# Optimization experiments

Measured on AMD Instinct MI355X. Metric: run time of the kernel, lower is better.

Reference implementation:

```python
import jax, jax.numpy as jnp
import numpy as np

B = 128
E, IN, H, OUT, ZD = 6, 1664, 512, 618, 32


def setup_inputs() -> dict:
    key = jax.random.key(0)
    ks = jax.random.split(key, 9)
    scale = 0.05
    return {
        "p_prev": jax.random.normal(ks[0], (B, IN), dtype=jnp.float32),
        "blending_coef": jax.random.uniform(ks[1], (B, E), dtype=jnp.float32),
        "z": jax.random.normal(ks[2], (B, ZD), dtype=jnp.float32),
        "w_l1": jax.random.normal(ks[3], (E, IN, H), dtype=jnp.float32) * scale,
        "b_l1": jax.random.normal(ks[4], (E, H), dtype=jnp.float32) * scale,
        "w_l2": jax.random.normal(ks[5], (E, H + ZD, H), dtype=jnp.float32) * scale,
        "b_l2": jax.random.normal(ks[6], (E, H + ZD, H)[0:0] + (E, H), dtype=jnp.float32) * scale,
        "w_l3": jax.random.normal(ks[7], (E, H + ZD, OUT), dtype=jnp.float32) * scale,
        "b_l3": jax.random.normal(ks[8], (E, OUT), dtype=jnp.float32) * scale,
    }


def _moe_layer(x, coef, w, b, use_act=True):
    # Per-sample blended weight matmul, fused as a single contraction:
    # y[b,o] = sum_i x[b,i] * (sum_e coef[b,e] * w[e,i,o]) + sum_e coef[b,e] * b[e,o]
    y = jnp.einsum("bi,eio,be->bo", x, w, coef) + jnp.einsum("be,eo->bo", coef, b)
    return jax.nn.elu(y) if use_act else y


def reference(p_prev, blending_coef, z, w_l1, b_l1, w_l2, b_l2, w_l3, b_l3):
    x = _moe_layer(p_prev, blending_coef, w_l1, b_l1)              # [B, H]
    x = _moe_layer(jnp.concatenate([x, z], axis=-1), blending_coef, w_l2, b_l2)  # [B, H]
    x = _moe_layer(jnp.concatenate([x, z], axis=-1), blending_coef, w_l3, b_l3, use_act=False)  # [B, OUT]
    return x
```

## Files before the change

### kernel.cpp

```cpp
#include <hip/hip_runtime.h>
#include <math.h>

#define B 128
#define E 6
#define IN_DIM 1664
#define H_DIM 512
#define OUT_DIM 618
#define ZD 32
#define K2 544
#define S1 26
#define S23 17

typedef __attribute__((ext_vector_type(8))) short short8;
typedef __attribute__((ext_vector_type(4))) float f32x4;
union U128 { uint4 u4; short8 s8; ushort us[8]; };

__device__ __forceinline__ ushort f2bf(float f) {
    uint u = __float_as_uint(f);
    u += 0x7fffu + ((u >> 16) & 1u);
    return (ushort)(u >> 16);
}
__device__ __forceinline__ uint pk2(float a, float b) {
    return (uint)f2bf(a) | ((uint)f2bf(b) << 16);
}
__device__ __forceinline__ float elu1(float x) { return x < 0.f ? expm1f(x) : x; }


__global__ __launch_bounds__(256) void init_bias(
    const float* __restrict__ coef,
    const float* __restrict__ b1, const float* __restrict__ b2,
    const float* __restrict__ b3,
    float* __restrict__ y1, float* __restrict__ y2, float* __restrict__ out)
{
    const int idx = blockIdx.x * 256 + threadIdx.x;
    if (idx >= B * (2 * H_DIM + OUT_DIM)) return;
    const int b = idx / (2 * H_DIM + OUT_DIM);
    const int o = idx - b * (2 * H_DIM + OUT_DIM);
    float ce[E];
    #pragma unroll
    for (int e = 0; e < E; ++e) ce[e] = coef[b * E + e];
    float v = 0.f;
    if (o < H_DIM) {
        #pragma unroll
        for (int e = 0; e < E; ++e) v = fmaf(ce[e], b1[e * H_DIM + o], v);
        y1[b * H_DIM + o] = v;
    } else if (o < 2 * H_DIM) {
        const int oo = o - H_DIM;
        #pragma unroll
        for (int e = 0; e < E; ++e) v = fmaf(ce[e], b2[e * H_DIM + oo], v);
        y2[b * H_DIM + oo] = v;
    } else {
        const int oo = o - 2 * H_DIM;
        #pragma unroll
        for (int e = 0; e < E; ++e) v = fmaf(ce[e], b3[e * OUT_DIM + oo], v);
        out[b * OUT_DIM + oo] = v;
    }
}

__global__ __launch_bounds__(256) void gemm1(
    const float* __restrict__ x,
    const float* __restrict__ coef,
    const float* __restrict__ w,
    float* __restrict__ y1)
{
    constexpr int NS = E * 2;
    const int tid = threadIdx.x;
    const int l = tid & 63, wv = tid >> 6;
    const int n0 = blockIdx.x * 16, kb0 = blockIdx.y * 2;
    const int tn = tid & 15, tq = tid >> 4;
    const int lp = ((tq >> 2) << 4) | tn;
    const int j0 = (2 * tq) & 7;
    const int row0 = 32 * wv + (l & 15), row1 = row0 + 16, kq = l >> 4;

    __shared__ ushort bs[NS][64][8];

    float wreg[NS][2];
    #pragma unroll
    for (int s = 0; s < NS; ++s) {
        const int e = s % E, kb = kb0 + s / E;
        const float* src = w + ((size_t)e * IN_DIM + kb * 32 + 2 * tq) * H_DIM + n0 + tn;
        wreg[s][0] = src[0];
        wreg[s][1] = src[H_DIM];
    }
    float4 xreg[2][4];
    #pragma unroll
    for (int kbi = 0; kbi < 2; ++kbi) {
        const float* p0 = x + (size_t)row0 * IN_DIM + (kb0 + kbi) * 32 + kq * 8;
        const float* p1 = x + (size_t)row1 * IN_DIM + (kb0 + kbi) * 32 + kq * 8;
        xreg[kbi][0] = *reinterpret_cast<const float4*>(p0);
        xreg[kbi][1] = *reinterpret_cast<const float4*>(p0 + 4);
        xreg[kbi][2] = *reinterpret_cast<const float4*>(p1);
        xreg[kbi][3] = *reinterpret_cast<const float4*>(p1 + 4);
    }
    float ce0[E], ce1[E];
    #pragma unroll
    for (int e = 0; e < E; ++e) {
        ce0[e] = coef[row0 * E + e];
        ce1[e] = coef[row1 * E + e];
    }

    #pragma unroll
    for (int s = 0; s < NS; ++s)
        *reinterpret_cast<uint*>(&bs[s][lp][j0]) = pk2(wreg[s][0], wreg[s][1]);
    __syncthreads();

    f32x4 acc0 = {0.f,0.f,0.f,0.f}, acc1 = {0.f,0.f,0.f,0.f};
    #pragma unroll
    for (int s = 0; s < NS; ++s) {
        const int e = s % E, kbi = s / E;
        const float4* xc = xreg[kbi];
        U128 a0, a1;
        a0.us[0] = f2bf(xc[0].x * ce0[e]); a0.us[1] = f2bf(xc[0].y * ce0[e]);
        a0.us[2] = f2bf(xc[0].z * ce0[e]); a0.us[3] = f2bf(xc[0].w * ce0[e]);
        a0.us[4] = f2bf(xc[1].x * ce0[e]); a0.us[5] = f2bf(xc[1].y * ce0[e]);
        a0.us[6] = f2bf(xc[1].z * ce0[e]); a0.us[7] = f2bf(xc[1].w * ce0[e]);
        a1.us[0] = f2bf(xc[2].x * ce1[e]); a1.us[1] = f2bf(xc[2].y * ce1[e]);
        a1.us[2] = f2bf(xc[2].z * ce1[e]); a1.us[3] = f2bf(xc[2].w * ce1[e]);
        a1.us[4] = f2bf(xc[3].x * ce1[e]); a1.us[5] = f2bf(xc[3].y * ce1[e]);
        a1.us[6] = f2bf(xc[3].z * ce1[e]); a1.us[7] = f2bf(xc[3].w * ce1[e]);

        U128 b0;
        b0.u4 = *reinterpret_cast<const uint4*>(&bs[s][l][0]);
        acc0 = __builtin_amdgcn_mfma_f32_16x16x32_bf16(a0.s8, b0.s8, acc0, 0, 0, 0);
        acc1 = __builtin_amdgcn_mfma_f32_16x16x32_bf16(a1.s8, b0.s8, acc1, 0, 0, 0);
    }

    const int colB = n0 + (l & 15);
    const int rsub = (l >> 4) << 2;
    #pragma unroll
    for (int mi = 0; mi < 2; ++mi) {
        const int row = wv * 32 + mi * 16 + rsub;
        const f32x4 c = mi ? acc1 : acc0;
        #pragma unroll
        for (int r = 0; r < 4; ++r)
            atomicAdd(&y1[(size_t)(row + r) * H_DIM + colB], c[r]);
    }
}

template<bool ZS, int NW, bool GUARD>
__device__ __forceinline__ void gemm_mid_body(
    const float* __restrict__ yin,
    const float* __restrict__ coef,
    const float* __restrict__ z,
    const float* __restrict__ w,
    float* __restrict__ yout,
    int nt, int kb0, ushort (*bs)[64][8])
{
    constexpr int NS = E;
    const int tid = threadIdx.x;
    const int l = tid & 63, wv = tid >> 6;
    const int n0 = nt * 16;
    const int tn = tid & 15, tq = tid >> 4;
    const int lp = ((tq >> 2) << 4) | tn;
    const int j0 = (2 * tq) & 7;
    const int row0 = 32 * wv + (l & 15), row1 = row0 + 16, kq = l >> 4;
    const bool okS = !GUARD || (n0 + tn) < NW;
    const bool okC = !GUARD || (n0 + (l & 15)) < NW;

    float wreg[NS][2];
    #pragma unroll
    for (int s = 0; s < NS; ++s) {
        const float* src = w + ((size_t)s * K2 + kb0 * 32 + 2 * tq) * NW + n0 + tn;
        wreg[s][0] = okS ? src[0] : 0.f;
        wreg[s][1] = okS ? src[NW] : 0.f;
    }

    float ce0[E], ce1[E];
    #pragma unroll
    for (int e = 0; e < E; ++e) {
        ce0[e] = coef[row0 * E + e];
        ce1[e] = coef[row1 * E + e];
    }

    float v0[8], v1[8];
    if (ZS) {
        const float4 za = *reinterpret_cast<const float4*>(z + row0 * ZD + kq * 8);
        const float4 zb = *reinterpret_cast<const float4*>(z + row0 * ZD + kq * 8 + 4);
        const float4 zc = *reinterpret_cast<const float4*>(z + row1 * ZD + kq * 8);
        const float4 zd = *reinterpret_cast<const float4*>(z + row1 * ZD + kq * 8 + 4);
        v0[0]=za.x; v0[1]=za.y; v0[2]=za.z; v0[3]=za.w;
        v0[4]=zb.x; v0[5]=zb.y; v0[6]=zb.z; v0[7]=zb.w;
        v1[0]=zc.x; v1[1]=zc.y; v1[2]=zc.z; v1[3]=zc.w;
        v1[4]=zd.x; v1[5]=zd.y; v1[6]=zd.z; v1[7]=zd.w;
    } else {
        const int kk = kb0 * 32 + kq * 8;
        const float* p0 = yin + (size_t)row0 * H_DIM + kk;
        const float* p1 = yin + (size_t)row1 * H_DIM + kk;
        const float4 a = *reinterpret_cast<const float4*>(p0);
        const float4 b = *reinterpret_cast<const float4*>(p0 + 4);
        const float4 c = *reinterpret_cast<const float4*>(p1);
        const float4 d = *reinterpret_cast<const float4*>(p1 + 4);
        v0[0]=elu1(a.x); v0[1]=elu1(a.y); v0[2]=elu1(a.z); v0[3]=elu1(a.w);
        v0[4]=elu1(b.x); v0[5]=elu1(b.y); v0[6]=elu1(b.z); v0[7]=elu1(b.w);
        v1[0]=elu1(c.x); v1[1]=elu1(c.y); v1[2]=elu1(c.z); v1[3]=elu1(c.w);
        v1[4]=elu1(d.x); v1[5]=elu1(d.y); v1[6]=elu1(d.z); v1[7]=elu1(d.w);
    }

    #pragma unroll
    for (int s = 0; s < NS; ++s)
        *reinterpret_cast<uint*>(&bs[s][lp][j0]) = pk2(wreg[s][0], wreg[s][1]);
    __syncthreads();

    f32x4 acc0 = {0.f,0.f,0.f,0.f}, acc1 = {0.f,0.f,0.f,0.f};
    #pragma unroll
    for (int s = 0; s < NS; ++s) {
        U128 a0, a1;
        #pragma unroll
        for (int j = 0; j < 8; ++j) {
            a0.us[j] = f2bf(v0[j] * ce0[s]);
            a1.us[j] = f2bf(v1[j] * ce1[s]);
        }
        U128 b0;
        b0.u4 = *reinterpret_cast<const uint4*>(&bs[s][l][0]);
        acc0 = __builtin_amdgcn_mfma_f32_16x16x32_bf16(a0.s8, b0.s8, acc0, 0, 0, 0);
        acc1 = __builtin_amdgcn_mfma_f32_16x16x32_bf16(a1.s8, b0.s8, acc1, 0, 0, 0);
    }

    const int colB = n0 + (l & 15);
    const int rsub = (l >> 4) << 2;
    #pragma unroll
    for (int mi = 0; mi < 2; ++mi) {
        const int row = wv * 32 + mi * 16 + rsub;
        const f32x4 c = mi ? acc1 : acc0;
        #pragma unroll
        for (int r = 0; r < 4; ++r)
            if (okC) atomicAdd(&yout[(size_t)(row + r) * NW + colB], c[r]);
    }
}

__global__ __launch_bounds__(256) void gemm_l2(
    const float* __restrict__ y1, const float* __restrict__ coef,
    const float* __restrict__ z, const float* __restrict__ w2,
    float* __restrict__ y2)
{
    __shared__ ushort bs[E][64][8];
    const int nt = blockIdx.x, sp = blockIdx.y;
    if (sp < 16)
        gemm_mid_body<false, H_DIM, false>(y1, coef, z, w2, y2, nt, sp, bs);
    else
        gemm_mid_body<true, H_DIM, false>(y1, coef, z, w2, y2, nt, 16, bs);
}

__global__ __launch_bounds__(256) void gemm_l3(
    const float* __restrict__ y2, const float* __restrict__ coef,
    const float* __restrict__ z, const float* __restrict__ w3,
    float* __restrict__ out)
{
    __shared__ ushort bs[E][64][8];
    const int nt = blockIdx.x, sp = blockIdx.y;
    if (sp < 16)
        gemm_mid_body<false, OUT_DIM, true>(y2, coef, z, w3, out, nt, sp, bs);
    else
        gemm_mid_body<true, OUT_DIM, true>(y2, coef, z, w3, out, nt, 16, bs);
}

extern "C" void kernel_launch(void* const* d_in, const int* in_sizes, int n_in,
                              void* d_out, int out_size, void* d_ws, size_t ws_size,
                              hipStream_t stream)
{
    const float* p_prev = (const float*)d_in[0];
    const float* coef   = (const float*)d_in[1];
    const float* z      = (const float*)d_in[2];
    const float* w1     = (const float*)d_in[3];
    const float* b1     = (const float*)d_in[4];
    const float* w2     = (const float*)d_in[5];
    const float* b2     = (const float*)d_in[6];
    const float* w3     = (const float*)d_in[7];
    const float* b3     = (const float*)d_in[8];
    float* out = (float*)d_out;

    float* y1 = (float*)d_ws;
    float* y2 = y1 + (size_t)B * H_DIM;

    const int TOT = B * (2 * H_DIM + OUT_DIM);
    init_bias<<<(TOT + 255) / 256, 256, 0, stream>>>(coef, b1, b2, b3, y1, y2, out);
    gemm1<<<dim3(32, S1), 256, 0, stream>>>(p_prev, coef, w1, y1);
    gemm_l2<<<dim3(32, S23), 256, 0, stream>>>(y1, coef, z, w2, y2);
    gemm_l3<<<dim3(39, S23), 256, 0, stream>>>(y2, coef, z, w3, out);
}
```

Before: 47.21 us.

## Split batch rows across blocks, deepen K per block, fold bias init into gemm1

Each block now covers 64 batch rows instead of all 128, with one MFMA chain per wave, and handles more K slices per block (4 k-blocks in gemm1, 2 in layers 2 and 3). This halves the split-K fan-out of atomics per output while doubling the column-tile grid. Bias init for y2 and out moves into an extra row of gemm1 blocks, leaving a small vectorized init kernel for y1. The trade-off is that each weight tile is now loaded twice (once per row half), which raises weight traffic, and each block uses more registers for the deeper K slice.

```diff
diff --git a/kernel.cpp b/kernel.cpp
--- a/kernel.cpp
+++ b/kernel.cpp
@@ -8,8 +8,6 @@
 #define OUT_DIM 618
 #define ZD 32
 #define K2 544
-#define S1 26
-#define S23 17
 
 typedef __attribute__((ext_vector_type(8))) short short8;
 typedef __attribute__((ext_vector_type(4))) float f32x4;
@@ -26,205 +24,188 @@
 __device__ __forceinline__ float elu1(float x) { return x < 0.f ? expm1f(x) : x; }
 
 
-__global__ __launch_bounds__(256) void init_bias(
-    const float* __restrict__ coef,
-    const float* __restrict__ b1, const float* __restrict__ b2,
-    const float* __restrict__ b3,
-    float* __restrict__ y1, float* __restrict__ y2, float* __restrict__ out)
-{
-    const int idx = blockIdx.x * 256 + threadIdx.x;
-    if (idx >= B * (2 * H_DIM + OUT_DIM)) return;
-    const int b = idx / (2 * H_DIM + OUT_DIM);
-    const int o = idx - b * (2 * H_DIM + OUT_DIM);
-    float ce[E];
-    #pragma unroll
-    for (int e = 0; e < E; ++e) ce[e] = coef[b * E + e];
-    float v = 0.f;
-    if (o < H_DIM) {
-        #pragma unroll
-        for (int e = 0; e < E; ++e) v = fmaf(ce[e], b1[e * H_DIM + o], v);
-        y1[b * H_DIM + o] = v;
-    } else if (o < 2 * H_DIM) {
-        const int oo = o - H_DIM;
-        #pragma unroll
-        for (int e = 0; e < E; ++e) v = fmaf(ce[e], b2[e * H_DIM + oo], v);
-        y2[b * H_DIM + oo] = v;
-    } else {
-        const int oo = o - 2 * H_DIM;
-        #pragma unroll
-        for (int e = 0; e < E; ++e) v = fmaf(ce[e], b3[e * OUT_DIM + oo], v);
-        out[b * OUT_DIM + oo] = v;
-    }
+__global__ __launch_bounds__(256) void init_y1(
+    const float* __restrict__ coef, const float* __restrict__ b1,
+    float* __restrict__ y1)
+{
+    const int t = blockIdx.x * 256 + threadIdx.x;
+    const int b = t >> 7, o = (t & 127) << 2;
+    float4 v = {0.f, 0.f, 0.f, 0.f};
+    #pragma unroll
+    for (int e = 0; e < E; ++e) {
+        const float c = coef[b * E + e];
+        const float4 bb = *reinterpret_cast<const float4*>(b1 + e * H_DIM + o);
+        v.x = fmaf(c, bb.x, v.x); v.y = fmaf(c, bb.y, v.y);
+        v.z = fmaf(c, bb.z, v.z); v.w = fmaf(c, bb.w, v.w);
+    }
+    *reinterpret_cast<float4*>(y1 + b * H_DIM + o) = v;
 }
 
 __global__ __launch_bounds__(256) void gemm1(
     const float* __restrict__ x,
     const float* __restrict__ coef,
     const float* __restrict__ w,
-    float* __restrict__ y1)
-{
-    constexpr int NS = E * 2;
+    const float* __restrict__ b2, const float* __restrict__ b3,
+    float* __restrict__ y1, float* __restrict__ y2, float* __restrict__ out)
+{
+    __shared__ ushort bs[24][64][8];
     const int tid = threadIdx.x;
+
+    if (blockIdx.y == 0) {
+        const int t = blockIdx.x * 256 + tid;
+        {
+            const int b = t >> 7, o = (t & 127) << 2;
+            float4 v = {0.f, 0.f, 0.f, 0.f};
+            #pragma unroll
+            for (int e = 0; e < E; ++e) {
+                const float c = coef[b * E + e];
+                const float4 bb = *reinterpret_cast<const float4*>(b2 + e * H_DIM + o);
+                v.x = fmaf(c, bb.x, v.x); v.y = fmaf(c, bb.y, v.y);
+                v.z = fmaf(c, bb.z, v.z); v.w = fmaf(c, bb.w, v.w);
+            }
+            *reinterpret_cast<float4*>(y2 + b * H_DIM + o) = v;
+        }
+        for (int i = t; i < B * OUT_DIM; i += 64 * 256) {
+            const int b = i / OUT_DIM, o = i - b * OUT_DIM;
+            float v = 0.f;
+            #pragma unroll
+            for (int e = 0; e < E; ++e)
+                v = fmaf(coef[b * E + e], b3[e * OUT_DIM + o], v);
+            out[i] = v;
+        }
+        return;
+    }
+
+    const int kb0 = (blockIdx.y - 1) * 4;
+    const int n0 = (blockIdx.x & 31) * 16, rowbase = (blockIdx.x >> 5) * 64;
     const int l = tid & 63, wv = tid >> 6;
-    const int n0 = blockIdx.x * 16, kb0 = blockIdx.y * 2;
     const int tn = tid & 15, tq = tid >> 4;
-    const int lp = ((tq >> 2) << 4) | tn;
-    const int j0 = (2 * tq) & 7;
-    const int row0 = 32 * wv + (l & 15), row1 = row0 + 16, kq = l >> 4;
-
-    __shared__ ushort bs[NS][64][8];
-
-    float wreg[NS][2];
-    #pragma unroll
-    for (int s = 0; s < NS; ++s) {
-        const int e = s % E, kb = kb0 + s / E;
-        const float* src = w + ((size_t)e * IN_DIM + kb * 32 + 2 * tq) * H_DIM + n0 + tn;
-        wreg[s][0] = src[0];
-        wreg[s][1] = src[H_DIM];
-    }
-    float4 xreg[2][4];
-    #pragma unroll
-    for (int kbi = 0; kbi < 2; ++kbi) {
-        const float* p0 = x + (size_t)row0 * IN_DIM + (kb0 + kbi) * 32 + kq * 8;
-        const float* p1 = x + (size_t)row1 * IN_DIM + (kb0 + kbi) * 32 + kq * 8;
-        xreg[kbi][0] = *reinterpret_cast<const float4*>(p0);
-        xreg[kbi][1] = *reinterpret_cast<const float4*>(p0 + 4);
-        xreg[kbi][2] = *reinterpret_cast<const float4*>(p1);
-        xreg[kbi][3] = *reinterpret_cast<const float4*>(p1 + 4);
-    }
-    float ce0[E], ce1[E];
-    #pragma unroll
-    for (int e = 0; e < E; ++e) {
-        ce0[e] = coef[row0 * E + e];
-        ce1[e] = coef[row1 * E + e];
-    }
-
-    #pragma unroll
-    for (int s = 0; s < NS; ++s)
-        *reinterpret_cast<uint*>(&bs[s][lp][j0]) = pk2(wreg[s][0], wreg[s][1]);
+    const int lp = ((tq >> 2) << 4) | tn, j0 = (2 * tq) & 7;
+    const int row = rowbase + wv * 16 + (l & 15);
+    const int kq = l >> 4;
+
+    float ce[E];
+    #pragma unroll
+    for (int e = 0; e < E; ++e) ce[e] = coef[row * E + e];
+
+    float xv[4][8];
+    #pragma unroll
+    for (int kbi = 0; kbi < 4; ++kbi) {
+        const float* p = x + (size_t)row * IN_DIM + (kb0 + kbi) * 32 + kq * 8;
+        const float4 a = *reinterpret_cast<const float4*>(p);
+        const float4 b = *reinterpret_cast<const float4*>(p + 4);
+        xv[kbi][0] = a.x; xv[kbi][1] = a.y; xv[kbi][2] = a.z; xv[kbi][3] = a.w;
+        xv[kbi][4] = b.x; xv[kbi][5] = b.y; xv[kbi][6] = b.z; xv[kbi][7] = b.w;
+    }
+
+    #pragma unroll
+    for (int bb = 0; bb < 2; ++bb) {
+        float wr[12][2];
+        #pragma unroll
+        for (int ss = 0; ss < 12; ++ss) {
+            const int s = bb * 12 + ss;
+            const int e = s % E, kb = kb0 + s / E;
+            const float* src = w + ((size_t)e * IN_DIM + kb * 32 + 2 * tq) * H_DIM + n0 + tn;
+            wr[ss][0] = src[0];
+            wr[ss][1] = src[H_DIM];
+        }
+        #pragma unroll
+        for (int ss = 0; ss < 12; ++ss)
+            *reinterpret_cast<uint*>(&bs[bb * 12 + ss][lp][j0]) =
+                pk2(wr[ss][0], wr[ss][1]);
+    }
     __syncthreads();
 
-    f32x4 acc0 = {0.f,0.f,0.f,0.f}, acc1 = {0.f,0.f,0.f,0.f};
-    #pragma unroll
-    for (int s = 0; s < NS; ++s) {
+    f32x4 acc = {0.f, 0.f, 0.f, 0.f};
+    #pragma unroll
+    for (int s = 0; s < 24; ++s) {
         const int e = s % E, kbi = s / E;
-        const float4* xc = xreg[kbi];
-        U128 a0, a1;
-        a0.us[0] = f2bf(xc[0].x * ce0[e]); a0.us[1] = f2bf(xc[0].y * ce0[e]);
-        a0.us[2] = f2bf(xc[0].z * ce0[e]); a0.us[3] = f2bf(xc[0].w * ce0[e]);
-        a0.us[4] = f2bf(xc[1].x * ce0[e]); a0.us[5] = f2bf(xc[1].y * ce0[e]);
-        a0.us[6] = f2bf(xc[1].z * ce0[e]); a0.us[7] = f2bf(xc[1].w * ce0[e]);
-        a1.us[0] = f2bf(xc[2].x * ce1[e]); a1.us[1] = f2bf(xc[2].y * ce1[e]);
-        a1.us[2] = f2bf(xc[2].z * ce1[e]); a1.us[3] = f2bf(xc[2].w * ce1[e]);
-        a1.us[4] = f2bf(xc[3].x * ce1[e]); a1.us[5] = f2bf(xc[3].y * ce1[e]);
-        a1.us[6] = f2bf(xc[3].z * ce1[e]); a1.us[7] = f2bf(xc[3].w * ce1[e]);
-
-        U128 b0;
+        U128 a, b0;
+        #pragma unroll
+        for (int j = 0; j < 8; ++j) a.us[j] = f2bf(xv[kbi][j] * ce[e]);
         b0.u4 = *reinterpret_cast<const uint4*>(&bs[s][l][0]);
-        acc0 = __builtin_amdgcn_mfma_f32_16x16x32_bf16(a0.s8, b0.s8, acc0, 0, 0, 0);
-        acc1 = __builtin_amdgcn_mfma_f32_16x16x32_bf16(a1.s8, b0.s8, acc1, 0, 0, 0);
+        acc = __builtin_amdgcn_mfma_f32_16x16x32_bf16(a.s8, b0.s8, acc, 0, 0, 0);
     }
 
     const int colB = n0 + (l & 15);
-    const int rsub = (l >> 4) << 2;
-    #pragma unroll
-    for (int mi = 0; mi < 2; ++mi) {
-        const int row = wv * 32 + mi * 16 + rsub;
-        const f32x4 c = mi ? acc1 : acc0;
-        #pragma unroll
-        for (int r = 0; r < 4; ++r)
-            atomicAdd(&y1[(size_t)(row + r) * H_DIM + colB], c[r]);
-    }
-}
-
-template<bool ZS, int NW, bool GUARD>
+    const int rowE = rowbase + wv * 16 + ((l >> 4) << 2);
+    #pragma unroll
+    for (int r = 0; r < 4; ++r)
+        atomicAdd(&y1[(size_t)(rowE + r) * H_DIM + colB], acc[r]);
+}
+
+template<int KPB, bool ZS, int NW, bool GUARD>
 __device__ __forceinline__ void gemm_mid_body(
     const float* __restrict__ yin,
     const float* __restrict__ coef,
     const float* __restrict__ z,
     const float* __restrict__ w,
     float* __restrict__ yout,
-    int nt, int kb0, ushort (*bs)[64][8])
-{
-    constexpr int NS = E;
+    int n0, int rowbase, int kb0, ushort (*bs)[64][8])
+{
+    constexpr int NS = E * KPB;
     const int tid = threadIdx.x;
     const int l = tid & 63, wv = tid >> 6;
-    const int n0 = nt * 16;
     const int tn = tid & 15, tq = tid >> 4;
-    const int lp = ((tq >> 2) << 4) | tn;
-    const int j0 = (2 * tq) & 7;
-    const int row0 = 32 * wv + (l & 15), row1 = row0 + 16, kq = l >> 4;
+    const int lp = ((tq >> 2) << 4) | tn, j0 = (2 * tq) & 7;
+    const int row = rowbase + wv * 16 + (l & 15);
+    const int kq = l >> 4;
     const bool okS = !GUARD || (n0 + tn) < NW;
-    const bool okC = !GUARD || (n0 + (l & 15)) < NW;
-
-    float wreg[NS][2];
+
+    float wr[NS][2];
     #pragma unroll
     for (int s = 0; s < NS; ++s) {
-        const float* src = w + ((size_t)s * K2 + kb0 * 32 + 2 * tq) * NW + n0 + tn;
-        wreg[s][0] = okS ? src[0] : 0.f;
-        wreg[s][1] = okS ? src[NW] : 0.f;
-    }
-
-    float ce0[E], ce1[E];
-    #pragma unroll
-    for (int e = 0; e < E; ++e) {
-        ce0[e] = coef[row0 * E + e];
-        ce1[e] = coef[row1 * E + e];
-    }
-
-    float v0[8], v1[8];
+        const int e = s % E, kb = kb0 + s / E;
+        const float* src = w + ((size_t)e * K2 + kb * 32 + 2 * tq) * NW + n0 + tn;
+        wr[s][0] = okS ? src[0] : 0.f;
+        wr[s][1] = okS ? src[NW] : 0.f;
+    }
+
+    float ce[E];
+    #pragma unroll
+    for (int e = 0; e < E; ++e) ce[e] = coef[row * E + e];
+
+    float v[KPB * 8];
     if (ZS) {
-        const float4 za = *reinterpret_cast<const float4*>(z + row0 * ZD + kq * 8);
-        const float4 zb = *reinterpret_cast<const float4*>(z + row0 * ZD + kq * 8 + 4);
-        const float4 zc = *reinterpret_cast<const float4*>(z + row1 * ZD + kq * 8);
-        const float4 zd = *reinterpret_cast<const float4*>(z + row1 * ZD + kq * 8 + 4);
-        v0[0]=za.x; v0[1]=za.y; v0[2]=za.z; v0[3]=za.w;
-        v0[4]=zb.x; v0[5]=zb.y; v0[6]=zb.z; v0[7]=zb.w;
-        v1[0]=zc.x; v1[1]=zc.y; v1[2]=zc.z; v1[3]=zc.w;
-        v1[4]=zd.x; v1[5]=zd.y; v1[6]=zd.z; v1[7]=zd.w;
+        const float4 a = *reinterpret_cast<const float4*>(z + row * ZD + kq * 8);
+        const float4 b = *reinterpret_cast<const float4*>(z + row * ZD + kq * 8 + 4);
+        v[0] = a.x; v[1] = a.y; v[2] = a.z; v[3] = a.w;
+        v[4] = b.x; v[5] = b.y; v[6] = b.z; v[7] = b.w;
     } else {
-        const int kk = kb0 * 32 + kq * 8;
-        const float* p0 = yin + (size_t)row0 * H_DIM + kk;
-        const float* p1 = yin + (size_t)row1 * H_DIM + kk;
-        const float4 a = *reinterpret_cast<const float4*>(p0);
-        const float4 b = *reinterpret_cast<const float4*>(p0 + 4);
-        const float4 c = *reinterpret_cast<const float4*>(p1);
-        const float4 d = *reinterpret_cast<const float4*>(p1 + 4);
-        v0[0]=elu1(a.x); v0[1]=elu1(a.y); v0[2]=elu1(a.z); v0[3]=elu1(a.w);
-        v0[4]=elu1(b.x); v0[5]=elu1(b.y); v0[6]=elu1(b.z); v0[7]=elu1(b.w);
-        v1[0]=elu1(c.x); v1[1]=elu1(c.y); v1[2]=elu1(c.z); v1[3]=elu1(c.w);
-        v1[4]=elu1(d.x); v1[5]=elu1(d.y); v1[6]=elu1(d.z); v1[7]=elu1(d.w);
+        #pragma unroll
+        for (int kbi = 0; kbi < KPB; ++kbi) {
+            const float* p = yin + (size_t)row * H_DIM + (kb0 + kbi) * 32 + kq * 8;
+            const float4 a = *reinterpret_cast<const float4*>(p);
+            const float4 b = *reinterpret_cast<const float4*>(p + 4);
+            v[kbi*8+0] = elu1(a.x); v[kbi*8+1] = elu1(a.y);
+            v[kbi*8+2] = elu1(a.z); v[kbi*8+3] = elu1(a.w);
+            v[kbi*8+4] = elu1(b.x); v[kbi*8+5] = elu1(b.y);
+            v[kbi*8+6] = elu1(b.z); v[kbi*8+7] = elu1(b.w);
+        }
     }
 
     #pragma unroll
     for (int s = 0; s < NS; ++s)
-        *reinterpret_cast<uint*>(&bs[s][lp][j0]) = pk2(wreg[s][0], wreg[s][1]);
+        *reinterpret_cast<uint*>(&bs[s][lp][j0]) = pk2(wr[s][0], wr[s][1]);
     __syncthreads();
 
-    f32x4 acc0 = {0.f,0.f,0.f,0.f}, acc1 = {0.f,0.f,0.f,0.f};
+    f32x4 acc = {0.f, 0.f, 0.f, 0.f};
     #pragma unroll
     for (int s = 0; s < NS; ++s) {
-        U128 a0, a1;
-        #pragma unroll
-        for (int j = 0; j < 8; ++j) {
-            a0.us[j] = f2bf(v0[j] * ce0[s]);
-            a1.us[j] = f2bf(v1[j] * ce1[s]);
-        }
-        U128 b0;
+        const int e = s % E, kbi = s / E;
+        U128 a, b0;
+        #pragma unroll
+        for (int j = 0; j < 8; ++j) a.us[j] = f2bf(v[kbi * 8 + j] * ce[e]);
         b0.u4 = *reinterpret_cast<const uint4*>(&bs[s][l][0]);
-        acc0 = __builtin_amdgcn_mfma_f32_16x16x32_bf16(a0.s8, b0.s8, acc0, 0, 0, 0);
-        acc1 = __builtin_amdgcn_mfma_f32_16x16x32_bf16(a1.s8, b0.s8, acc1, 0, 0, 0);
+        acc = __builtin_amdgcn_mfma_f32_16x16x32_bf16(a.s8, b0.s8, acc, 0, 0, 0);
     }
 
     const int colB = n0 + (l & 15);
-    const int rsub = (l >> 4) << 2;
-    #pragma unroll
-    for (int mi = 0; mi < 2; ++mi) {
-        const int row = wv * 32 + mi * 16 + rsub;
-        const f32x4 c = mi ? acc1 : acc0;
+    const int rowE = rowbase + wv * 16 + ((l >> 4) << 2);
+    if (!GUARD || colB < NW) {
         #pragma unroll
         for (int r = 0; r < 4; ++r)
-            if (okC) atomicAdd(&yout[(size_t)(row + r) * NW + colB], c[r]);
+            atomicAdd(&yout[(size_t)(rowE + r) * NW + colB], acc[r]);
     }
 }
 
@@ -233,12 +214,15 @@
     const float* __restrict__ z, const float* __restrict__ w2,
     float* __restrict__ y2)
 {
-    __shared__ ushort bs[E][64][8];
-    const int nt = blockIdx.x, sp = blockIdx.y;
-    if (sp < 16)
-        gemm_mid_body<false, H_DIM, false>(y1, coef, z, w2, y2, nt, sp, bs);
+    __shared__ ushort bs[12][64][8];
+    const int n0 = (blockIdx.x & 31) * 16, rowbase = (blockIdx.x >> 5) * 64;
+    const int sp = blockIdx.y;
+    if (sp < 8)
+        gemm_mid_body<2, false, H_DIM, false>(y1, coef, z, w2, y2,
+                                              n0, rowbase, sp * 2, bs);
     else
-        gemm_mid_body<true, H_DIM, false>(y1, coef, z, w2, y2, nt, 16, bs);
+        gemm_mid_body<1, true, H_DIM, false>(y1, coef, z, w2, y2,
+                                             n0, rowbase, 16, bs);
 }
 
 __global__ __launch_bounds__(256) void gemm_l3(
@@ -246,12 +230,16 @@
     const float* __restrict__ z, const float* __restrict__ w3,
     float* __restrict__ out)
 {
-    __shared__ ushort bs[E][64][8];
-    const int nt = blockIdx.x, sp = blockIdx.y;
-    if (sp < 16)
-        gemm_mid_body<false, OUT_DIM, true>(y2, coef, z, w3, out, nt, sp, bs);
+    __shared__ ushort bs[12][64][8];
+    const int nt = blockIdx.x % 40, rt = blockIdx.x / 40;
+    const int n0 = nt * 16, rowbase = rt * 64;
+    const int sp = blockIdx.y;
+    if (sp < 8)
+        gemm_mid_body<2, false, OUT_DIM, true>(y2, coef, z, w3, out,
+                                               n0, rowbase, sp * 2, bs);
     else
-        gemm_mid_body<true, OUT_DIM, true>(y2, coef, z, w3, out, nt, 16, bs);
+        gemm_mid_body<1, true, OUT_DIM, true>(y2, coef, z, w3, out,
+                                              n0, rowbase, 16, bs);
 }
 
 extern "C" void kernel_launch(void* const* d_in, const int* in_sizes, int n_in,
@@ -272,9 +260,9 @@
     float* y1 = (float*)d_ws;
     float* y2 = y1 + (size_t)B * H_DIM;
 
-    const int TOT = B * (2 * H_DIM + OUT_DIM);
-    init_bias<<<(TOT + 255) / 256, 256, 0, stream>>>(coef, b1, b2, b3, y1, y2, out);
-    gemm1<<<dim3(32, S1), 256, 0, stream>>>(p_prev, coef, w1, y1);
-    gemm_l2<<<dim3(32, S23), 256, 0, stream>>>(y1, coef, z, w2, y2);
-    gemm_l3<<<dim3(39, S23), 256, 0, stream>>>(y2, coef, z, w3, out);
-}
+    init_y1<<<64, 256, 0, stream>>>(coef, b1, y1);
+    gemm1<<<dim3(64, 14), 256, 0, stream>>>(p_prev, coef, w1, b2, b3,
+                                            y1, y2, out);
+    gemm_l2<<<dim3(64, 9), 256, 0, stream>>>(y1, coef, z, w2, y2);
+    gemm_l3<<<dim3(80, 9), 256, 0, stream>>>(y2, coef, z, w3, out);
+}
```

Result: faster. 41.46 us (-12.2%).
